# Performance work log

Hardware: AMD Instinct MI355X
Metric: run time of the kernel (lower is better)

## Reference

```python
import jax, jax.numpy as jnp
import numpy as np
import math

B, S, D = 1, 4096, 2048
H, KVH, HD = 16, 4, 128
ROPE_THETA = 10000.0


def _rope_tables(seq_len, head_dim, theta):
    inv_freq = 1.0 / (theta ** (jnp.arange(0, head_dim, 2, dtype=jnp.float32) / head_dim))
    t = jnp.arange(seq_len, dtype=jnp.float32)
    freqs = jnp.outer(t, inv_freq)                      # [S, HD/2]
    emb = jnp.concatenate([freqs, freqs], axis=-1)      # [S, HD]
    return jnp.cos(emb)[None, None], jnp.sin(emb)[None, None]  # [1,1,S,HD]


def setup_inputs() -> dict:
    key = jax.random.key(0)
    ks = jax.random.split(key, 8)
    hidden_states = jax.random.normal(ks[0], (B, S, D), dtype=jnp.float32)
    # additive causal mask [B,1,S,S]
    neg = jnp.finfo(jnp.float32).min
    causal = jnp.where(jnp.tril(jnp.ones((S, S), dtype=bool)), 0.0, neg)
    attention_mask = jnp.broadcast_to(causal[None, None], (B, 1, S, S)).astype(jnp.float32)
    cos, sin = _rope_tables(S, HD, ROPE_THETA)
    gate = jax.random.uniform(ks[1], (B, S), dtype=jnp.float32, minval=0.05, maxval=1.0)
    sc = lambda fan_in: 1.0 / math.sqrt(fan_in)
    Wq = jax.random.normal(ks[2], (D, H * HD), dtype=jnp.float32) * sc(D)
    Wk = jax.random.normal(ks[3], (D, KVH * HD), dtype=jnp.float32) * sc(D)
    Wv = jax.random.normal(ks[4], (D, KVH * HD), dtype=jnp.float32) * sc(D)
    Wo = jax.random.normal(ks[5], (H * HD, D), dtype=jnp.float32) * sc(H * HD)
    return {"hidden_states": hidden_states, "attention_mask": attention_mask,
            "cos": cos, "sin": sin, "gate": gate,
            "Wq": Wq, "Wk": Wk, "Wv": Wv, "Wo": Wo}


def _rotate_half(x):
    h = x.shape[-1] // 2
    return jnp.concatenate([-x[..., h:], x[..., :h]], axis=-1)


def reference(hidden_states, attention_mask, cos, sin, gate, Wq, Wk, Wv, Wo):
    bsz, q_len, _ = hidden_states.shape
    # projections -> [B, heads, S, HD]
    q = (hidden_states @ Wq).reshape(bsz, q_len, H, HD).transpose(0, 2, 1, 3)
    k = (hidden_states @ Wk).reshape(bsz, q_len, KVH, HD).transpose(0, 2, 1, 3)
    v = (hidden_states @ Wv).reshape(bsz, q_len, KVH, HD).transpose(0, 2, 1, 3)
    # inline RoPE
    q = q * cos + _rotate_half(q) * sin
    k = k * cos + _rotate_half(k) * sin
    # GQA: repeat-interleave kv heads to match q heads
    g = H // KVH
    k = jnp.repeat(k, g, axis=1)
    v = jnp.repeat(v, g, axis=1)
    scores = jnp.einsum('bhqd,bhkd->bhqk', q, k) / math.sqrt(HD)
    scores = scores + attention_mask
    scores = scores + jnp.log(gate + 1e-8)[:, None, None, :]  # gate over kv positions
    weights = jax.nn.softmax(scores.astype(jnp.float32), axis=-1).astype(q.dtype)
    out = jnp.einsum('bhqk,bhkd->bhqd', weights, v)
    out = out.transpose(0, 2, 1, 3).reshape(bsz, q_len, H * HD)
    return out @ Wo
```

## Files before the change

kernel.cpp:

```cpp
#include <hip/hip_runtime.h>
#include <math.h>

#define S_LEN 4096
#define DMODEL 2048
#define NH 16
#define NKVH 4
#define HD 128
#define LDQKV 3072

typedef __attribute__((ext_vector_type(4))) float f32x4;
typedef __attribute__((ext_vector_type(8))) short bf16x8;
typedef __attribute__((ext_vector_type(4))) unsigned short us4;

static __device__ __forceinline__ unsigned short f2bf(float f) {
  unsigned int u = __builtin_bit_cast(unsigned int, f);
  u += 0x7fffu + ((u >> 16) & 1u);
  return (unsigned short)(u >> 16);
}
static __device__ __forceinline__ float bf2f(unsigned short h) {
  unsigned int u = ((unsigned int)h) << 16;
  return __builtin_bit_cast(float, u);
}
static __device__ __forceinline__ unsigned int cvt_pk_bf16(float lo, float hi) {
  unsigned int r;
  asm("v_cvt_pk_bf16_f32 %0, %1, %2" : "=v"(r) : "v"(lo), "v"(hi));
  return r;
}

#define GLDS16(g, l) __builtin_amdgcn_global_load_lds( \
    (__attribute__((address_space(1))) void*)(g), \
    (__attribute__((address_space(3))) void*)(l), 16, 0, 0)


__global__ __launch_bounds__(256) void k_prep(
    const float* __restrict__ hid, unsigned short* __restrict__ Xb,
    const float* __restrict__ Wq, const float* __restrict__ Wk,
    const float* __restrict__ Wv, const float* __restrict__ Wo,
    unsigned short* __restrict__ Wt, unsigned short* __restrict__ Wot) {
  __shared__ float tile[64][65];
  const int b = blockIdx.x, t = threadIdx.x;
  if (b < 8192) {
    int i = b * 256 + t;
    const float4* s = (const float4*)hid;
    float4 v = s[i];
    us4 o = { f2bf(v.x), f2bf(v.y), f2bf(v.z), f2bf(v.w) };
    *(us4*)(Xb + (size_t)i * 4) = o;
    return;
  }
  const int bb = b - 8192;
  const float* src;
  unsigned short* dst;
  int N, c;
  if (bb < 1024)      { src = Wq; dst = Wt;                       N = 2048; c = bb; }
  else if (bb < 1280) { src = Wk; dst = Wt + (size_t)2048 * 2048; N = 512;  c = bb - 1024; }
  else if (bb < 1536) { src = Wv; dst = Wt + (size_t)2560 * 2048; N = 512;  c = bb - 1280; }
  else                { src = Wo; dst = Wot;                      N = 2048; c = bb - 1536; }
  const int k0 = (c & 31) * 64, n0 = (c >> 5) * 64;
#pragma unroll
  for (int i = 0; i < 16; ++i) {
    int idx = t + i * 256;
    int r = idx >> 6, cc = idx & 63;
    tile[r][cc] = src[(size_t)(k0 + r) * N + n0 + cc];
  }
  __syncthreads();
#pragma unroll
  for (int i = 0; i < 16; ++i) {
    int idx = t + i * 256;
    int r = idx >> 6, cc = idx & 63;
    dst[(size_t)(n0 + r) * 2048 + k0 + cc] = f2bf(tile[cc][r]);
  }
}


__global__ __launch_bounds__(256) void k_vt(
    const unsigned short* __restrict__ QKV, unsigned short* __restrict__ Vt) {
  __shared__ unsigned short tile[64][72];
  const int b = blockIdx.x, t = threadIdx.x;
  const int s0 = (b & 63) * 64, c0 = (b >> 6) * 64;
#pragma unroll
  for (int i = 0; i < 16; ++i) {
    int idx = t + i * 256;
    int r = idx >> 6, cc = idx & 63;
    tile[r][cc] = QKV[(size_t)(s0 + r) * LDQKV + DMODEL + NKVH * HD + c0 + cc];
  }
  __syncthreads();
#pragma unroll
  for (int i = 0; i < 16; ++i) {
    int idx = t + i * 256;
    int r = idx >> 6, cc = idx & 63;
    int pc = (cc & 3) * 16 + (cc >> 2);
    Vt[(size_t)(c0 + r) * S_LEN + s0 + cc] = tile[pc][r];
  }
}


template<int MODE>
__global__ __launch_bounds__(256) void k_gemm_bt(
    const unsigned short* __restrict__ A, const unsigned short* __restrict__ Bt,
    void* __restrict__ Cp, int M, int N, int K,
    const float* __restrict__ cp, const float* __restrict__ sp) {
  __shared__ __attribute__((aligned(16))) unsigned short As[128 * 32];
  __shared__ __attribute__((aligned(16))) unsigned short Bs[128 * 32];
  const int t = threadIdx.x;
  const int wave = t >> 6, lane = t & 63;
  const int lr = lane & 15, lg = lane >> 4;
  const int bm = blockIdx.x * 128, bn = blockIdx.y * 128;
  const int wr = wave * 32;
  f32x4 acc[2][8];
#pragma unroll
  for (int i = 0; i < 2; ++i)
#pragma unroll
    for (int j = 0; j < 8; ++j) acc[i][j] = (f32x4){0.f, 0.f, 0.f, 0.f};

  for (int k0 = 0; k0 < K; k0 += 32) {
    __syncthreads();
#pragma unroll
    for (int i = 0; i < 2; ++i) {
      const int cb = (wave * 2 + i) * 64;
      const int c = cb + lane;
      const int row = c >> 2, kc = c & 3;
      const int ksw = (kc ^ (row & 3)) * 8;
      GLDS16(A + (size_t)(bm + row) * K + k0 + ksw, (char*)As + cb * 16);
      GLDS16(Bt + (size_t)(bn + row) * K + k0 + ksw, (char*)Bs + cb * 16);
    }
    asm volatile("s_waitcnt vmcnt(0)" ::: "memory");
    __syncthreads();
    bf16x8 af[2], bfr[8];
#pragma unroll
    for (int mi = 0; mi < 2; ++mi) {
      const int row = wr + mi * 16 + lr;
      af[mi] = *(const bf16x8*)(As + row * 32 + ((lg ^ (lr & 3)) * 8));
    }
#pragma unroll
    for (int ni = 0; ni < 8; ++ni) {
      const int row = ni * 16 + lr;
      bfr[ni] = *(const bf16x8*)(Bs + row * 32 + ((lg ^ (lr & 3)) * 8));
    }
#pragma unroll
    for (int mi = 0; mi < 2; ++mi)
#pragma unroll
      for (int ni = 0; ni < 8; ++ni)
        acc[mi][ni] = __builtin_amdgcn_mfma_f32_16x16x32_bf16(af[mi], bfr[ni], acc[mi][ni], 0, 0, 0);
  }

  if (MODE == 1 && bn < NKVH * HD + DMODEL) {
    const float qs = bn < DMODEL ? 0.12751589341664477f : 1.0f;
    unsigned short* o = (unsigned short*)Cp;
#pragma unroll
    for (int mi = 0; mi < 2; ++mi)
#pragma unroll
      for (int r = 0; r < 4; ++r) {
        const int m = bm + wr + mi * 16 + lg * 4 + r;
#pragma unroll
        for (int ni = 0; ni < 4; ++ni) {
          const int d = ni * 16 + lr;
          const float c = cp[m * HD + d], s = sp[m * HD + d];
          const float x1 = acc[mi][ni][r], x2 = acc[mi][ni + 4][r];
          o[(size_t)m * N + bn + d]      = f2bf((x1 * c - x2 * s) * qs);
          o[(size_t)m * N + bn + d + 64] = f2bf((x2 * c + x1 * s) * qs);
        }
      }
    return;
  }
#pragma unroll
  for (int mi = 0; mi < 2; ++mi)
#pragma unroll
    for (int ni = 0; ni < 8; ++ni)
#pragma unroll
      for (int r = 0; r < 4; ++r) {
        const int m = bm + wr + mi * 16 + lg * 4 + r;
        const int n = bn + ni * 16 + lr;
        if (MODE == 2) ((float*)Cp)[(size_t)m * N + n] = acc[mi][ni][r];
        else ((unsigned short*)Cp)[(size_t)m * N + n] = f2bf(acc[mi][ni][r]);
      }
}


#define STAGE_KV(kt_, buf_) do { \
  const int kv0_ = (kt_) * 128; \
  _Pragma("unroll") \
  for (int i_ = 0; i_ < 4; ++i_) { \
    const int cb_ = (wave * 4 + i_) * 64; \
    const int c_ = cb_ + lane; \
    const int row_ = c_ >> 4, kc_ = c_ & 15; \
    const int sw_ = (kc_ ^ (row_ & 7)) * 8; \
    GLDS16(Kp + (size_t)(kv0_ + row_) * LDQKV + sw_, (char*)Ks[buf_] + cb_ * 16); \
    GLDS16(Vp + (size_t)row_ * S_LEN + kv0_ + sw_, (char*)Vs[buf_] + cb_ * 16); \
  } \
} while (0)

__device__ __forceinline__ void qkt_one(const unsigned short* Kb,
    const bf16x8* qf, f32x4* sc, int lr, int lg) {
  __builtin_amdgcn_s_setprio(1);
#pragma unroll
  for (int cf = 0; cf < 8; ++cf) {
    sc[cf] = (f32x4){0.f, 0.f, 0.f, 0.f};
    const int row = cf * 16 + lr;
#pragma unroll
    for (int ks = 0; ks < 4; ++ks) {
      bf16x8 kb = *(const bf16x8*)(Kb + row * 128 + (((ks * 4 + lg) ^ (lr & 7)) * 8));
      sc[cf] = __builtin_amdgcn_mfma_f32_16x16x32_bf16(qf[ks], kb, sc[cf], 0, 0, 0);
    }
  }
  __builtin_amdgcn_s_setprio(0);
}

template<bool DIAG>
__device__ __forceinline__ void softmax_pv(
    f32x4* sc, const unsigned short* Vb, unsigned short (*PsW)[72],
    const float* g8, int kv0, int qbase,
    f32x4* acc, f32x4& acc_s, float* mrow, int lr, int lg,
    const bf16x8 vb_ones) {
  if (DIAG) {
#pragma unroll
    for (int cf = 0; cf < 8; ++cf) {
      const int kpos = kv0 + cf * 16 + lr;
#pragma unroll
      for (int r = 0; r < 4; ++r)
        sc[cf][r] = (kpos <= qbase + r) ? sc[cf][r] : -3e38f;
    }
  }
  float lmax[4];
#pragma unroll
  for (int r = 0; r < 4; ++r) {
    float a = fmaxf(fmaxf(sc[0][r], sc[1][r]), fmaxf(sc[2][r], sc[3][r]));
    float b = fmaxf(fmaxf(sc[4][r], sc[5][r]), fmaxf(sc[6][r], sc[7][r]));
    lmax[r] = fmaxf(a, b);
  }
  bool need = (lmax[0] > mrow[0] + 11.5416f) | (lmax[1] > mrow[1] + 11.5416f) |
              (lmax[2] > mrow[2] + 11.5416f) | (lmax[3] > mrow[3] + 11.5416f);
  if (__any(need)) {
    float tm[4] = {lmax[0], lmax[1], lmax[2], lmax[3]};
#pragma unroll
    for (int off = 8; off; off >>= 1)
#pragma unroll
      for (int r = 0; r < 4; ++r) tm[r] = fmaxf(tm[r], __shfl_xor(tm[r], off));
#pragma unroll
    for (int r = 0; r < 4; ++r) {
      const float mn = fmaxf(mrow[r], tm[r]);
      const float alpha = __builtin_amdgcn_exp2f(mrow[r] - mn);
      mrow[r] = mn;
#pragma unroll
      for (int j = 0; j < 8; ++j) acc[j][r] *= alpha;
      acc_s[r] *= alpha;
    }
  }
#pragma unroll
  for (int hh = 0; hh < 2; ++hh) {
    const f32x4* s4 = sc + hh * 4;
    const float* g4 = g8 + hh * 4;
#pragma unroll
    for (int r = 0; r < 4; ++r) {
      float p0 = __builtin_amdgcn_exp2f(s4[0][r] - mrow[r]) * g4[0];
      float p1 = __builtin_amdgcn_exp2f(s4[1][r] - mrow[r]) * g4[1];
      float p2 = __builtin_amdgcn_exp2f(s4[2][r] - mrow[r]) * g4[2];
      float p3 = __builtin_amdgcn_exp2f(s4[3][r] - mrow[r]) * g4[3];
      uint2 pk = { cvt_pk_bf16(p0, p1), cvt_pk_bf16(p2, p3) };
      *(uint2*)(&PsW[lg * 4 + r][lr * 4]) = pk;
    }
    __builtin_amdgcn_s_setprio(1);
#pragma unroll
    for (int ks = 0; ks < 2; ++ks) {
      bf16x8 pa = *(const bf16x8*)(&PsW[lr][ks * 32 + lg * 8]);
#pragma unroll
      for (int j = 0; j < 8; ++j) {
        const int d = j * 16 + lr;
        bf16x8 vb = *(const bf16x8*)(Vb + d * 128 + ((hh * 8 + ((ks * 4 + lg) ^ (lr & 7))) * 8));
        acc[j] = __builtin_amdgcn_mfma_f32_16x16x32_bf16(pa, vb, acc[j], 0, 0, 0);
      }
      acc_s = __builtin_amdgcn_mfma_f32_16x16x32_bf16(pa, vb_ones, acc_s, 0, 0, 0);
    }
    __builtin_amdgcn_s_setprio(0);
  }
}

__global__ __launch_bounds__(512) void k_attn(
    const unsigned short* __restrict__ QKV, const unsigned short* __restrict__ Vt,
    const float* __restrict__ gate, unsigned short* __restrict__ Oattn) {
  __shared__ __attribute__((aligned(16))) unsigned short Ks[2][128 * 128];
  __shared__ __attribute__((aligned(16))) unsigned short Vs[2][128 * 128];
  __shared__ __attribute__((aligned(16))) unsigned short Ps[8][16][72];
  const int h = blockIdx.y, kvh = h >> 2;
  const int bx = blockIdx.x;
  const int t = threadIdx.x, wave = t >> 6, lane = t & 63;
  const int lr = lane & 15, lg = lane >> 4;
  const unsigned short* Qp = QKV + h * HD;
  const unsigned short* Kp = QKV + DMODEL + kvh * HD;
  const unsigned short* Vp = Vt + (size_t)kvh * HD * S_LEN;
  unsigned short (*PsW)[72] = Ps[wave];
  bf16x8 vb_ones;
  {
    const short one = (short)0x3F80, z = 0;
    const short e = (lr == 0) ? one : z;
    vb_ones = (bf16x8){e, e, e, e, e, e, e, e};
  }

  for (int half = 0; half < 2; ++half) {
    const int st = half ? bx : (31 - bx);
    const int q0 = st * 128;
    const int nt = st + 1;
    const int qbase = q0 + wave * 16 + lg * 4;

    bf16x8 qf[4];
    {
      const size_t qoff = (size_t)(q0 + wave * 16 + lr) * LDQKV;
#pragma unroll
      for (int ks = 0; ks < 4; ++ks)
        qf[ks] = *(const bf16x8*)(Qp + qoff + ks * 32 + lg * 8);
    }
    f32x4 acc[8];
#pragma unroll
    for (int j = 0; j < 8; ++j) acc[j] = (f32x4){0.f, 0.f, 0.f, 0.f};
    f32x4 acc_s = (f32x4){0.f, 0.f, 0.f, 0.f};
    float mrow[4] = {-3e38f, -3e38f, -3e38f, -3e38f};
    f32x4 sc[8];
    float g8[8];

    __builtin_amdgcn_s_barrier();
    STAGE_KV(0, 0);

    int kt = 0;
    for (; kt < nt - 1; ++kt) {
      STAGE_KV(kt + 1, (kt + 1) & 1);
      asm volatile("s_waitcnt vmcnt(8)" ::: "memory");
      __builtin_amdgcn_s_barrier();
#pragma unroll
      for (int cf = 0; cf < 8; ++cf) g8[cf] = gate[kt * 128 + cf * 16 + lr];
      qkt_one(Ks[kt & 1], qf, sc, lr, lg);
      softmax_pv<false>(sc, Vs[kt & 1], PsW, g8, kt * 128, qbase, acc, acc_s, mrow, lr, lg, vb_ones);
      __builtin_amdgcn_s_barrier();
    }
    {
      asm volatile("s_waitcnt vmcnt(0)" ::: "memory");
      __builtin_amdgcn_s_barrier();
#pragma unroll
      for (int cf = 0; cf < 8; ++cf) g8[cf] = gate[kt * 128 + cf * 16 + lr];
      qkt_one(Ks[kt & 1], qf, sc, lr, lg);
      softmax_pv<true>(sc, Vs[kt & 1], PsW, g8, kt * 128, qbase, acc, acc_s, mrow, lr, lg, vb_ones);
    }

    float inv[4];
#pragma unroll
    for (int r = 0; r < 4; ++r)
      inv[r] = 1.0f / __shfl(acc_s[r], lane & 48);
#pragma unroll
    for (int j = 0; j < 8; ++j)
#pragma unroll
      for (int r = 0; r < 4; ++r)
        Oattn[(size_t)(qbase + r) * DMODEL + h * HD + j * 16 + lr] = f2bf(acc[j][r] * inv[r]);
  }
}


extern "C" void kernel_launch(void* const* d_in, const int* in_sizes, int n_in,
                              void* d_out, int out_size, void* d_ws, size_t ws_size,
                              hipStream_t stream) {
  (void)in_sizes; (void)n_in; (void)out_size; (void)ws_size;
  const float* hid  = (const float*)d_in[0];
  const float* cosp = (const float*)d_in[2];
  const float* sinp = (const float*)d_in[3];
  const float* gate = (const float*)d_in[4];
  const float* Wq   = (const float*)d_in[5];
  const float* Wk   = (const float*)d_in[6];
  const float* Wv   = (const float*)d_in[7];
  const float* Wo   = (const float*)d_in[8];
  float* out = (float*)d_out;
  char* ws = (char*)d_ws;
  unsigned short* Xb   = (unsigned short*)(ws);
  unsigned short* Wt   = (unsigned short*)(ws + (size_t)16777216);
  unsigned short* Wot  = (unsigned short*)(ws + (size_t)29360128);
  unsigned short* QKV  = (unsigned short*)(ws + (size_t)37748736);
  unsigned short* Oatt = (unsigned short*)(ws + (size_t)62914560);
  unsigned short* Vt   = (unsigned short*)(ws + (size_t)79691776);

  k_prep<<<10752, 256, 0, stream>>>(hid, Xb, Wq, Wk, Wv, Wo, Wt, Wot);
  k_gemm_bt<1><<<dim3(32, 24), 256, 0, stream>>>(Xb, Wt, QKV, 4096, 3072, 2048, cosp, sinp);
  k_vt<<<512, 256, 0, stream>>>(QKV, Vt);
  k_attn<<<dim3(16, 16), 512, 0, stream>>>(QKV, Vt, gate, Oatt);
  k_gemm_bt<2><<<dim3(32, 16), 256, 0, stream>>>(Oatt, Wot, out, 4096, 2048, 2048, nullptr, nullptr);
}
```

Measured before the change: 248.5 us.

## Process two query groups per wave with 64-wide KV tiles

Each wave now handles 32 query rows in two 16-row groups and shares each K/V fragment load across both groups' MFMAs. The KV tile shrinks from 128 to 64 keys, which halves the LDS staging buffers, and each block covers 256 query rows. The causal mask is applied only on tiles at or past the diagonal. The earlier pairing of a short and a long query tile per block is dropped, so per-block work is now strongly unbalanced across the causal triangle, and the longest block does roughly twice the per-wave work.

```diff
diff --git a/kernel.cpp b/kernel.cpp
--- a/kernel.cpp
+++ b/kernel.cpp
@@ -177,117 +177,32 @@
 
 
 #define STAGE_KV(kt_, buf_) do { \
-  const int kv0_ = (kt_) * 128; \
+  const int kv0_ = (kt_) * 64; \
   _Pragma("unroll") \
-  for (int i_ = 0; i_ < 4; ++i_) { \
-    const int cb_ = (wave * 4 + i_) * 64; \
+  for (int i_ = 0; i_ < 2; ++i_) { \
+    const int cb_ = (wave * 2 + i_) * 64; \
     const int c_ = cb_ + lane; \
-    const int row_ = c_ >> 4, kc_ = c_ & 15; \
-    const int sw_ = (kc_ ^ (row_ & 7)) * 8; \
-    GLDS16(Kp + (size_t)(kv0_ + row_) * LDQKV + sw_, (char*)Ks[buf_] + cb_ * 16); \
-    GLDS16(Vp + (size_t)row_ * S_LEN + kv0_ + sw_, (char*)Vs[buf_] + cb_ * 16); \
+    { const int row_ = c_ >> 4, kc_ = c_ & 15; \
+      GLDS16(Kp + (size_t)(kv0_ + row_) * LDQKV + ((kc_ ^ (row_ & 7)) * 8), \
+             (char*)Ks[buf_] + cb_ * 16); } \
+    { const int d_ = c_ >> 3, kc_ = c_ & 7; \
+      GLDS16(Vp + (size_t)d_ * S_LEN + kv0_ + ((kc_ ^ (d_ & 7)) * 8), \
+             (char*)Vs[buf_] + cb_ * 16); } \
   } \
 } while (0)
-
-__device__ __forceinline__ void qkt_one(const unsigned short* Kb,
-    const bf16x8* qf, f32x4* sc, int lr, int lg) {
-  __builtin_amdgcn_s_setprio(1);
-#pragma unroll
-  for (int cf = 0; cf < 8; ++cf) {
-    sc[cf] = (f32x4){0.f, 0.f, 0.f, 0.f};
-    const int row = cf * 16 + lr;
-#pragma unroll
-    for (int ks = 0; ks < 4; ++ks) {
-      bf16x8 kb = *(const bf16x8*)(Kb + row * 128 + (((ks * 4 + lg) ^ (lr & 7)) * 8));
-      sc[cf] = __builtin_amdgcn_mfma_f32_16x16x32_bf16(qf[ks], kb, sc[cf], 0, 0, 0);
-    }
-  }
-  __builtin_amdgcn_s_setprio(0);
-}
-
-template<bool DIAG>
-__device__ __forceinline__ void softmax_pv(
-    f32x4* sc, const unsigned short* Vb, unsigned short (*PsW)[72],
-    const float* g8, int kv0, int qbase,
-    f32x4* acc, f32x4& acc_s, float* mrow, int lr, int lg,
-    const bf16x8 vb_ones) {
-  if (DIAG) {
-#pragma unroll
-    for (int cf = 0; cf < 8; ++cf) {
-      const int kpos = kv0 + cf * 16 + lr;
-#pragma unroll
-      for (int r = 0; r < 4; ++r)
-        sc[cf][r] = (kpos <= qbase + r) ? sc[cf][r] : -3e38f;
-    }
-  }
-  float lmax[4];
-#pragma unroll
-  for (int r = 0; r < 4; ++r) {
-    float a = fmaxf(fmaxf(sc[0][r], sc[1][r]), fmaxf(sc[2][r], sc[3][r]));
-    float b = fmaxf(fmaxf(sc[4][r], sc[5][r]), fmaxf(sc[6][r], sc[7][r]));
-    lmax[r] = fmaxf(a, b);
-  }
-  bool need = (lmax[0] > mrow[0] + 11.5416f) | (lmax[1] > mrow[1] + 11.5416f) |
-              (lmax[2] > mrow[2] + 11.5416f) | (lmax[3] > mrow[3] + 11.5416f);
-  if (__any(need)) {
-    float tm[4] = {lmax[0], lmax[1], lmax[2], lmax[3]};
-#pragma unroll
-    for (int off = 8; off; off >>= 1)
-#pragma unroll
-      for (int r = 0; r < 4; ++r) tm[r] = fmaxf(tm[r], __shfl_xor(tm[r], off));
-#pragma unroll
-    for (int r = 0; r < 4; ++r) {
-      const float mn = fmaxf(mrow[r], tm[r]);
-      const float alpha = __builtin_amdgcn_exp2f(mrow[r] - mn);
-      mrow[r] = mn;
-#pragma unroll
-      for (int j = 0; j < 8; ++j) acc[j][r] *= alpha;
-      acc_s[r] *= alpha;
-    }
-  }
-#pragma unroll
-  for (int hh = 0; hh < 2; ++hh) {
-    const f32x4* s4 = sc + hh * 4;
-    const float* g4 = g8 + hh * 4;
-#pragma unroll
-    for (int r = 0; r < 4; ++r) {
-      float p0 = __builtin_amdgcn_exp2f(s4[0][r] - mrow[r]) * g4[0];
-      float p1 = __builtin_amdgcn_exp2f(s4[1][r] - mrow[r]) * g4[1];
-      float p2 = __builtin_amdgcn_exp2f(s4[2][r] - mrow[r]) * g4[2];
-      float p3 = __builtin_amdgcn_exp2f(s4[3][r] - mrow[r]) * g4[3];
-      uint2 pk = { cvt_pk_bf16(p0, p1), cvt_pk_bf16(p2, p3) };
-      *(uint2*)(&PsW[lg * 4 + r][lr * 4]) = pk;
-    }
-    __builtin_amdgcn_s_setprio(1);
-#pragma unroll
-    for (int ks = 0; ks < 2; ++ks) {
-      bf16x8 pa = *(const bf16x8*)(&PsW[lr][ks * 32 + lg * 8]);
-#pragma unroll
-      for (int j = 0; j < 8; ++j) {
-        const int d = j * 16 + lr;
-        bf16x8 vb = *(const bf16x8*)(Vb + d * 128 + ((hh * 8 + ((ks * 4 + lg) ^ (lr & 7))) * 8));
-        acc[j] = __builtin_amdgcn_mfma_f32_16x16x32_bf16(pa, vb, acc[j], 0, 0, 0);
-      }
-      acc_s = __builtin_amdgcn_mfma_f32_16x16x32_bf16(pa, vb_ones, acc_s, 0, 0, 0);
-    }
-    __builtin_amdgcn_s_setprio(0);
-  }
-}
 
 __global__ __launch_bounds__(512) void k_attn(
     const unsigned short* __restrict__ QKV, const unsigned short* __restrict__ Vt,
     const float* __restrict__ gate, unsigned short* __restrict__ Oattn) {
-  __shared__ __attribute__((aligned(16))) unsigned short Ks[2][128 * 128];
-  __shared__ __attribute__((aligned(16))) unsigned short Vs[2][128 * 128];
-  __shared__ __attribute__((aligned(16))) unsigned short Ps[8][16][72];
-  const int h = blockIdx.y, kvh = h >> 2;
-  const int bx = blockIdx.x;
+  __shared__ __attribute__((aligned(16))) unsigned short Ks[2][64 * 128];
+  __shared__ __attribute__((aligned(16))) unsigned short Vs[2][128 * 64];
+  __shared__ __attribute__((aligned(16))) unsigned short Ps[8][2][16][72];
+  const int st = blockIdx.x, h = blockIdx.y, kvh = h >> 2;
   const int t = threadIdx.x, wave = t >> 6, lane = t & 63;
   const int lr = lane & 15, lg = lane >> 4;
   const unsigned short* Qp = QKV + h * HD;
   const unsigned short* Kp = QKV + DMODEL + kvh * HD;
   const unsigned short* Vp = Vt + (size_t)kvh * HD * S_LEN;
-  unsigned short (*PsW)[72] = Ps[wave];
   bf16x8 vb_ones;
   {
     const short one = (short)0x3F80, z = 0;
@@ -295,59 +210,133 @@
     vb_ones = (bf16x8){e, e, e, e, e, e, e, e};
   }
 
-  for (int half = 0; half < 2; ++half) {
-    const int st = half ? bx : (31 - bx);
-    const int q0 = st * 128;
-    const int nt = st + 1;
-    const int qbase = q0 + wave * 16 + lg * 4;
-
-    bf16x8 qf[4];
-    {
-      const size_t qoff = (size_t)(q0 + wave * 16 + lr) * LDQKV;
-#pragma unroll
-      for (int ks = 0; ks < 4; ++ks)
-        qf[ks] = *(const bf16x8*)(Qp + qoff + ks * 32 + lg * 8);
-    }
-    f32x4 acc[8];
-#pragma unroll
-    for (int j = 0; j < 8; ++j) acc[j] = (f32x4){0.f, 0.f, 0.f, 0.f};
-    f32x4 acc_s = (f32x4){0.f, 0.f, 0.f, 0.f};
-    float mrow[4] = {-3e38f, -3e38f, -3e38f, -3e38f};
-    f32x4 sc[8];
-    float g8[8];
-
+  const int q0 = st * 256;
+  const int nt = 4 * st + 4;
+  const int qb[2] = { q0 + wave * 32 + lg * 4, q0 + wave * 32 + 16 + lg * 4 };
+
+  bf16x8 qf[2][4];
+#pragma unroll
+  for (int g = 0; g < 2; ++g) {
+    const size_t qoff = (size_t)(q0 + wave * 32 + g * 16 + lr) * LDQKV;
+#pragma unroll
+    for (int ks = 0; ks < 4; ++ks)
+      qf[g][ks] = *(const bf16x8*)(Qp + qoff + ks * 32 + lg * 8);
+  }
+  f32x4 acc[2][8];
+#pragma unroll
+  for (int g = 0; g < 2; ++g)
+#pragma unroll
+    for (int j = 0; j < 8; ++j) acc[g][j] = (f32x4){0.f, 0.f, 0.f, 0.f};
+  f32x4 acc_s[2] = { (f32x4){0.f, 0.f, 0.f, 0.f}, (f32x4){0.f, 0.f, 0.f, 0.f} };
+  float mrow[2][4] = { {-3e38f, -3e38f, -3e38f, -3e38f}, {-3e38f, -3e38f, -3e38f, -3e38f} };
+  f32x4 sc[2][4];
+  float g4[4];
+
+  STAGE_KV(0, 0);
+
+  for (int kt = 0; kt < nt; ++kt) {
+    const int kv0 = kt * 64;
+    if (kt + 1 < nt) {
+      STAGE_KV(kt + 1, (kt + 1) & 1);
+      asm volatile("s_waitcnt vmcnt(4)" ::: "memory");
+    } else {
+      asm volatile("s_waitcnt vmcnt(0)" ::: "memory");
+    }
     __builtin_amdgcn_s_barrier();
-    STAGE_KV(0, 0);
-
-    int kt = 0;
-    for (; kt < nt - 1; ++kt) {
-      STAGE_KV(kt + 1, (kt + 1) & 1);
-      asm volatile("s_waitcnt vmcnt(8)" ::: "memory");
-      __builtin_amdgcn_s_barrier();
-#pragma unroll
-      for (int cf = 0; cf < 8; ++cf) g8[cf] = gate[kt * 128 + cf * 16 + lr];
-      qkt_one(Ks[kt & 1], qf, sc, lr, lg);
-      softmax_pv<false>(sc, Vs[kt & 1], PsW, g8, kt * 128, qbase, acc, acc_s, mrow, lr, lg, vb_ones);
-      __builtin_amdgcn_s_barrier();
-    }
-    {
-      asm volatile("s_waitcnt vmcnt(0)" ::: "memory");
-      __builtin_amdgcn_s_barrier();
-#pragma unroll
-      for (int cf = 0; cf < 8; ++cf) g8[cf] = gate[kt * 128 + cf * 16 + lr];
-      qkt_one(Ks[kt & 1], qf, sc, lr, lg);
-      softmax_pv<true>(sc, Vs[kt & 1], PsW, g8, kt * 128, qbase, acc, acc_s, mrow, lr, lg, vb_ones);
-    }
-
+    const unsigned short* Kb = Ks[kt & 1];
+    const unsigned short* Vb = Vs[kt & 1];
+#pragma unroll
+    for (int cf = 0; cf < 4; ++cf) g4[cf] = gate[kv0 + cf * 16 + lr];
+
+    __builtin_amdgcn_s_setprio(1);
+#pragma unroll
+    for (int cf = 0; cf < 4; ++cf) {
+      sc[0][cf] = (f32x4){0.f, 0.f, 0.f, 0.f};
+      sc[1][cf] = (f32x4){0.f, 0.f, 0.f, 0.f};
+      const int row = cf * 16 + lr;
+#pragma unroll
+      for (int ks = 0; ks < 4; ++ks) {
+        bf16x8 kb = *(const bf16x8*)(Kb + row * 128 + (((ks * 4 + lg) ^ (lr & 7)) * 8));
+        sc[0][cf] = __builtin_amdgcn_mfma_f32_16x16x32_bf16(qf[0][ks], kb, sc[0][cf], 0, 0, 0);
+        sc[1][cf] = __builtin_amdgcn_mfma_f32_16x16x32_bf16(qf[1][ks], kb, sc[1][cf], 0, 0, 0);
+      }
+    }
+    __builtin_amdgcn_s_setprio(0);
+
+    const bool tail = kv0 >= q0;
+#pragma unroll
+    for (int g = 0; g < 2; ++g) {
+      if (tail) {
+#pragma unroll
+        for (int cf = 0; cf < 4; ++cf) {
+          const int kpos = kv0 + cf * 16 + lr;
+#pragma unroll
+          for (int r = 0; r < 4; ++r)
+            sc[g][cf][r] = (kpos <= qb[g] + r) ? sc[g][cf][r] : -3e38f;
+        }
+      }
+      float lmax[4];
+#pragma unroll
+      for (int r = 0; r < 4; ++r)
+        lmax[r] = fmaxf(fmaxf(sc[g][0][r], sc[g][1][r]), fmaxf(sc[g][2][r], sc[g][3][r]));
+      bool need = (lmax[0] > mrow[g][0] + 11.5416f) | (lmax[1] > mrow[g][1] + 11.5416f) |
+                  (lmax[2] > mrow[g][2] + 11.5416f) | (lmax[3] > mrow[g][3] + 11.5416f);
+      if (__any(need)) {
+        float tm[4] = {lmax[0], lmax[1], lmax[2], lmax[3]};
+#pragma unroll
+        for (int off = 8; off; off >>= 1)
+#pragma unroll
+          for (int r = 0; r < 4; ++r) tm[r] = fmaxf(tm[r], __shfl_xor(tm[r], off));
+#pragma unroll
+        for (int r = 0; r < 4; ++r) {
+          const float mn = fmaxf(mrow[g][r], tm[r]);
+          const float alpha = __builtin_amdgcn_exp2f(mrow[g][r] - mn);
+          mrow[g][r] = mn;
+#pragma unroll
+          for (int j = 0; j < 8; ++j) acc[g][j][r] *= alpha;
+          acc_s[g][r] *= alpha;
+        }
+      }
+#pragma unroll
+      for (int r = 0; r < 4; ++r) {
+        float p0 = __builtin_amdgcn_exp2f(sc[g][0][r] - mrow[g][r]) * g4[0];
+        float p1 = __builtin_amdgcn_exp2f(sc[g][1][r] - mrow[g][r]) * g4[1];
+        float p2 = __builtin_amdgcn_exp2f(sc[g][2][r] - mrow[g][r]) * g4[2];
+        float p3 = __builtin_amdgcn_exp2f(sc[g][3][r] - mrow[g][r]) * g4[3];
+        uint2 pk = { cvt_pk_bf16(p0, p1), cvt_pk_bf16(p2, p3) };
+        *(uint2*)(&Ps[wave][g][lg * 4 + r][lr * 4]) = pk;
+      }
+    }
+    __builtin_amdgcn_s_setprio(1);
+#pragma unroll
+    for (int ks = 0; ks < 2; ++ks) {
+      bf16x8 pa0 = *(const bf16x8*)(&Ps[wave][0][lr][ks * 32 + lg * 8]);
+      bf16x8 pa1 = *(const bf16x8*)(&Ps[wave][1][lr][ks * 32 + lg * 8]);
+#pragma unroll
+      for (int j = 0; j < 8; ++j) {
+        const int d = j * 16 + lr;
+        bf16x8 vb = *(const bf16x8*)(Vb + d * 64 + (((ks * 4 + lg) ^ (lr & 7)) * 8));
+        acc[0][j] = __builtin_amdgcn_mfma_f32_16x16x32_bf16(pa0, vb, acc[0][j], 0, 0, 0);
+        acc[1][j] = __builtin_amdgcn_mfma_f32_16x16x32_bf16(pa1, vb, acc[1][j], 0, 0, 0);
+      }
+      acc_s[0] = __builtin_amdgcn_mfma_f32_16x16x32_bf16(pa0, vb_ones, acc_s[0], 0, 0, 0);
+      acc_s[1] = __builtin_amdgcn_mfma_f32_16x16x32_bf16(pa1, vb_ones, acc_s[1], 0, 0, 0);
+    }
+    __builtin_amdgcn_s_setprio(0);
+    __builtin_amdgcn_s_barrier();
+  }
+
+#pragma unroll
+  for (int g = 0; g < 2; ++g) {
     float inv[4];
 #pragma unroll
     for (int r = 0; r < 4; ++r)
-      inv[r] = 1.0f / __shfl(acc_s[r], lane & 48);
+      inv[r] = 1.0f / __shfl(acc_s[g][r], lane & 48);
 #pragma unroll
     for (int j = 0; j < 8; ++j)
 #pragma unroll
       for (int r = 0; r < 4; ++r)
-        Oattn[(size_t)(qbase + r) * DMODEL + h * HD + j * 16 + lr] = f2bf(acc[j][r] * inv[r]);
+        Oattn[(size_t)(qb[g] + r) * DMODEL + h * HD + j * 16 + lr] = f2bf(acc[g][j][r] * inv[r]);
   }
 }
 
```

Measured after the change: 303.4 us. 1.22x slower.
